# Kernel tuning notes

Measured on AMD Instinct MI355X. Metric: run time of the kernel, lower is better.

## Reference

```python
import jax, jax.numpy as jnp
import numpy as np

S, B, D, F = 2048, 8, 1024, 4096
EPS = 1e-5

def setup_inputs() -> dict:
    key = jax.random.key(0)
    ks = jax.random.split(key, 16)
    sc = lambda fan_in: 1.0 / np.sqrt(fan_in)
    inp = {
        'src': jax.random.normal(ks[0], (S, B, D), dtype=jnp.float32),
        'wq': jax.random.uniform(ks[1], (D, D), jnp.float32, -sc(D), sc(D)),
        'bq': jnp.zeros((D,), jnp.float32),
        'wk': jax.random.uniform(ks[2], (D, D), jnp.float32, -sc(D), sc(D)),
        'bk': jnp.zeros((D,), jnp.float32),
        'wv': jax.random.uniform(ks[3], (D, D), jnp.float32, -sc(D), sc(D)),
        'bv': jnp.zeros((D,), jnp.float32),
        'wo': jax.random.uniform(ks[4], (D, D), jnp.float32, -sc(D), sc(D)),
        'bo': jnp.zeros((D,), jnp.float32),
        'w1': jax.random.uniform(ks[5], (F, D), jnp.float32, -sc(D), sc(D)),
        'b1': jnp.zeros((F,), jnp.float32),
        'w2': jax.random.uniform(ks[6], (D, F), jnp.float32, -sc(F), sc(F)),
        'b2': jnp.zeros((D,), jnp.float32),
        'g1': jnp.ones((D,), jnp.float32),
        'be1': jnp.zeros((D,), jnp.float32),
        'g2': jnp.ones((D,), jnp.float32),
        'be2': jnp.zeros((D,), jnp.float32),
    }
    return inp

def _layer_norm(x, g, b):
    mu = jnp.mean(x, axis=-1, keepdims=True)
    var = jnp.mean(jnp.square(x - mu), axis=-1, keepdims=True)
    return (x - mu) / jnp.sqrt(var + EPS) * g + b

def _forward(src, wq, bq, wk, bk, wv, bv, wo, bo, w1, b1, w2, b2, g1, be1, g2, be2):
    # Linear attention (ELU+1 feature map, no normalizer — faithful to source)
    Q = jax.nn.elu(src @ wq.T + bq) + 1.0  # [S,B,D]
    K = jax.nn.elu(src @ wk.T + bk) + 1.0  # [S,B,D]
    V = src @ wv.T + bv                    # [S,B,D]
    KV = jnp.einsum('sbd,sbe->bde', K, V)  # [B,D,D]
    attn = jnp.einsum('sbd,bde->sbe', Q, KV)  # [S,B,D]
    attn = attn @ wo.T + bo
    x = _layer_norm(src + attn, g1, be1)   # dropout is identity (p=0 / eval)
    ffn = jax.nn.relu(x @ w1.T + b1) @ w2.T + b2
    return _layer_norm(x + ffn, g2, be2)

def reference(src, wq, bq, wk, bk, wv, bv, wo, bo, w1, b1, w2, b2, g1, be1, g2, be2):
    return _forward(src, wq, bq, wk, bk, wv, bv, wo, bo, w1, b1, w2, b2, g1, be1, g2, be2)
```

## Files before the change

### kernel.cpp

```cpp
#include <hip/hip_runtime.h>
#include <hip/hip_bf16.h>
#include <math.h>


typedef __attribute__((ext_vector_type(8))) short short8;
typedef __attribute__((ext_vector_type(4))) short short4_t;
typedef __attribute__((ext_vector_type(4))) float f32x4;

#define S_DIM 2048
#define B_DIM 8
#define D_DIM 1024
#define F_DIM 4096

__device__ __forceinline__ unsigned short f2bf(float f) {
  __hip_bfloat16 h = __float2bfloat16(f);
  return *reinterpret_cast<unsigned short*>(&h);
}
__device__ __forceinline__ float bf2f(unsigned short u) {
  return __bfloat162float(*reinterpret_cast<const __hip_bfloat16*>(&u));
}

#define GLD16(gp, sp)                                              \
  __builtin_amdgcn_global_load_lds(                                \
      (const __attribute__((address_space(1))) void*)(gp),         \
      (__attribute__((address_space(3))) void*)(sp), 16, 0, 0)

#define BAR()                                  \
  do {                                         \
    asm volatile("" ::: "memory");             \
    __builtin_amdgcn_s_barrier();              \
    asm volatile("" ::: "memory");             \
  } while (0)
#define WAITVM6() asm volatile("s_waitcnt vmcnt(6)" ::: "memory")
#define WAITVM10() asm volatile("s_waitcnt vmcnt(10)" ::: "memory")
#define WAITVM0() asm volatile("s_waitcnt vmcnt(0)" ::: "memory")

template <int EPI>
__global__ __launch_bounds__(512, 2) void gemm256_kernel(
    const unsigned short* __restrict__ A, long lda, long sA,
    const unsigned short* __restrict__ B, long ldb, long sB,
    void* __restrict__ Cv, long ldc, long sC,
    const float* __restrict__ bias,
    const void* __restrict__ residv, long ldr, long sR, int K) {
  __shared__ short lds[65536];
  const int gx = gridDim.x;
  const int nwg = gx * gridDim.y;
  const int orig = blockIdx.y * gx + blockIdx.x;
  const int cpx = nwg >> 3;
  const int wgid = (orig & 7) * cpx + (orig >> 3);
  const int bx = wgid % gx, by = wgid / gx;
  const int bz = blockIdx.z;
  const unsigned short* Ablk = A + (long)bz * sA + (long)by * 256 * lda;
  const unsigned short* Bblk = B + (long)bz * sB + (long)bx * 256 * ldb;

  const int tid = threadIdx.x;
  const int w = tid >> 6, lane = tid & 63;
  const int wm = w >> 2, wn = w & 3;
  const int lr = lane & 15, kh = lane >> 4;

  const int sr = w * 8 + (lane >> 3);
  const int sc = ((lane & 7) ^ (lane >> 3)) * 8;
  const int br0 = sr + ((sr >> 5) << 5);
  const unsigned short* pA = Ablk + (long)sr * lda + sc;
  const unsigned short* pB = Bblk + (long)br0 * ldb + sc;
  const long dA1 = 128 * lda, dAh = 64 * lda;
  const long dB1 = 128 * ldb, dBh = 32 * ldb;
  const int dst0 = w * 1024;
  const int dst1 = (8 + w) * 1024;

#define STAGE_A(bufOff, h, rel)                                               \
  do {                                                                        \
    GLD16(pA + (h) * dAh + (rel) * 64,                                        \
          (char*)lds + (bufOff) + (h)*16384 + dst0);                          \
    GLD16(pA + (h) * dAh + dA1 + (rel) * 64,                                  \
          (char*)lds + (bufOff) + (h)*16384 + dst1);                          \
  } while (0)
#define STAGE_B(bufOff, nh, rel)                                              \
  do {                                                                        \
    GLD16(pB + (nh) * dBh + (rel) * 64,                                       \
          (char*)lds + (bufOff) + 32768 + (nh)*16384 + dst0);                 \
    GLD16(pB + (nh) * dBh + dB1 + (rel) * 64,                                 \
          (char*)lds + (bufOff) + 32768 + (nh)*16384 + dst1);                 \
  } while (0)

  const int chk0 = ((kh ^ (lr & 7)) << 4);
  const int chk1 = (((4 + kh) ^ (lr & 7)) << 4);
  const int aRdBase = (wm * 64 + lr) * 128;
  const int bRdBase = (wn * 32 + lr) * 128;

  short8 af[4][2], b0r[2][2], b1r[2][2];
  f32x4 acc[8][4];
#pragma unroll
  for (int m = 0; m < 8; ++m)
#pragma unroll
    for (int n = 0; n < 4; ++n)
#pragma unroll
      for (int j = 0; j < 4; ++j) acc[m][n][j] = 0.f;

#define LDA_H(bufOff, h)                                                     \
  do {                                                                       \
    const char* _p = (const char*)lds + (bufOff) + (h)*16384 + aRdBase;      \
    _Pragma("unroll") for (int m = 0; m < 4; ++m) {                          \
      af[m][0] = *(const short8*)(_p + m * 2048 + chk0);                     \
      af[m][1] = *(const short8*)(_p + m * 2048 + chk1);                     \
    }                                                                        \
  } while (0)
#define LDB_H(dst, bufOff, nh)                                               \
  do {                                                                       \
    const char* _p = (const char*)lds + (bufOff) + 32768 + (nh)*16384 + bRdBase; \
    _Pragma("unroll") for (int n = 0; n < 2; ++n) {                          \
      dst[n][0] = *(const short8*)(_p + n * 2048 + chk0);                    \
      dst[n][1] = *(const short8*)(_p + n * 2048 + chk1);                    \
    }                                                                        \
  } while (0)
#define MFMA_Q(mh, nh, bset)                                                 \
  do {                                                                       \
    __builtin_amdgcn_s_setprio(1);                                           \
    _Pragma("unroll") for (int ks = 0; ks < 2; ++ks)                         \
    _Pragma("unroll") for (int m = 0; m < 4; ++m)                            \
    _Pragma("unroll") for (int n = 0; n < 2; ++n)                            \
      acc[(mh)*4 + m][(nh)*2 + n] = __builtin_amdgcn_mfma_f32_16x16x32_bf16( \
          af[m][ks], bset[n][ks], acc[(mh)*4 + m][(nh)*2 + n], 0, 0, 0);     \
    __builtin_amdgcn_s_setprio(0);                                           \
  } while (0)

  const int T = K >> 6;
  STAGE_A(0, 0, 0); STAGE_B(0, 0, 0); STAGE_B(0, 1, 0); STAGE_A(0, 1, 0);
  STAGE_A(65536, 0, 1); STAGE_B(65536, 0, 1); STAGE_B(65536, 1, 1);
  WAITVM10(); BAR();
  LDB_H(b0r, 0, 0);

  for (int i = 0; i < (T >> 1) - 1; ++i) {
    LDA_H(0, 0); STAGE_A(65536, 1, 1);
    BAR(); MFMA_Q(0, 0, b0r); BAR();
    LDB_H(b1r, 0, 1); STAGE_A(0, 0, 2);
    BAR(); MFMA_Q(0, 1, b1r); BAR();
    LDA_H(0, 1); STAGE_B(0, 0, 2);
    BAR(); MFMA_Q(1, 1, b1r); BAR();
    STAGE_B(0, 1, 2);
    WAITVM6(); BAR(); MFMA_Q(1, 0, b0r); LDB_H(b0r, 65536, 0); BAR();
    LDA_H(65536, 0); STAGE_A(0, 1, 2);
    BAR(); MFMA_Q(0, 0, b0r); BAR();
    LDB_H(b1r, 65536, 1); STAGE_A(65536, 0, 3);
    BAR(); MFMA_Q(0, 1, b1r); BAR();
    LDA_H(65536, 1); STAGE_B(65536, 0, 3);
    BAR(); MFMA_Q(1, 1, b1r); BAR();
    STAGE_B(65536, 1, 3);
    WAITVM6(); BAR(); MFMA_Q(1, 0, b0r); LDB_H(b0r, 0, 0); BAR();
    pA += 128; pB += 128;
  }

  LDA_H(0, 0); STAGE_A(65536, 1, 1);
  BAR(); MFMA_Q(0, 0, b0r); BAR();
  LDB_H(b1r, 0, 1);
  BAR(); MFMA_Q(0, 1, b1r); BAR();
  LDA_H(0, 1);
  BAR(); MFMA_Q(1, 1, b1r); BAR();
  WAITVM0(); BAR(); MFMA_Q(1, 0, b0r); LDB_H(b0r, 65536, 0); BAR();
  LDA_H(65536, 0);
  BAR(); MFMA_Q(0, 0, b0r); BAR();
  LDB_H(b1r, 65536, 1);
  BAR(); MFMA_Q(0, 1, b1r); BAR();
  LDA_H(65536, 1);
  BAR(); MFMA_Q(1, 1, b1r); BAR();
  MFMA_Q(1, 0, b0r);

  const long gm0 = (long)by * 256 + wm * 128;
  const long gn0 = (long)bx * 256 + wn * 64;
  if constexpr (EPI == 7) {
    unsigned short* C = (unsigned short*)Cv + (long)bz * sC;
    const float* R = (const float*)residv + (long)bz * sR;
#pragma unroll
    for (int mg = 0; mg < 8; ++mg)
#pragma unroll
      for (int ng = 0; ng < 4; ++ng) {
        const long col = gn0 + ng * 16 + lr;
        const float bcol = bias[col];
#pragma unroll
        for (int j = 0; j < 4; ++j) {
          const long row = gm0 + mg * 16 + kh * 4 + j;
          C[row * ldc + col] = f2bf(acc[mg][ng][j] + bcol + R[row * ldr + col]);
        }
      }
  } else if constexpr (EPI == 8) {
    unsigned short* C = (unsigned short*)Cv + (long)bz * sC;
    const unsigned short* R = (const unsigned short*)residv + (long)bz * sR;
#pragma unroll
    for (int mg = 0; mg < 8; ++mg)
#pragma unroll
      for (int ng = 0; ng < 4; ++ng) {
        const long col = gn0 + ng * 16 + lr;
        const float bcol = bias[col];
#pragma unroll
        for (int j = 0; j < 4; ++j) {
          const long row = gm0 + mg * 16 + kh * 4 + j;
          C[row * ldc + col] =
              f2bf(acc[mg][ng][j] + bcol + bf2f(R[row * ldr + col]));
        }
      }
  } else {
    unsigned short* C = (unsigned short*)Cv + (long)bz * sC;
    const bool do_elu = (EPI == 5) && (gn0 < 2048);
#pragma unroll
    for (int mg = 0; mg < 8; ++mg)
#pragma unroll
      for (int ng = 0; ng < 4; ++ng) {
        const long col = gn0 + ng * 16 + lr;
        float bcol = 0.f;
        if constexpr (EPI != 0) bcol = bias[col];
#pragma unroll
        for (int j = 0; j < 4; ++j) {
          const long row = gm0 + mg * 16 + kh * 4 + j;
          float v = acc[mg][ng][j] + bcol;
          if constexpr (EPI == 3) v = fmaxf(v, 0.f);
          if constexpr (EPI == 5) {
            if (do_elu) v = (v > 0.f) ? (v + 1.f) : expf(v);
          }
          C[row * ldc + col] = f2bf(v);
        }
      }
  }
#undef STAGE_A
#undef STAGE_B
#undef LDA_H
#undef LDB_H
#undef MFMA_Q
}

__global__ __launch_bounds__(256) void transpose_kernel(
    const unsigned short* __restrict__ inbase,
    unsigned short* __restrict__ outbase, long ld) {
  __shared__ unsigned short t[64][68];
  const int z = blockIdx.z;
  const int which = z >> 3, b = z & 7;
  const unsigned short* in = inbase + (which ? 2048 : 1024);
  unsigned short* out = outbase + (long)which * 16777216L;
  const long s0 = (long)blockIdx.x * 64, d0 = (long)blockIdx.y * 64;
  const int tid = threadIdx.x;
  {
    const int r = tid >> 3, c = (tid & 7) * 8;
#pragma unroll
    for (int it = 0; it < 2; ++it) {
      const int s = r + it * 32;
      const unsigned short* g = &in[((s0 + s) * B_DIM + b) * ld + d0 + c];
      short4_t v0 = *(const short4_t*)g;
      short4_t v1 = *(const short4_t*)(g + 4);
      *(short4_t*)&t[s][c] = v0;
      *(short4_t*)&t[s][c + 4] = v1;
    }
  }
  __syncthreads();
  {
    const int d = tid >> 3, c = (tid & 7) * 8;
#pragma unroll
    for (int it = 0; it < 2; ++it) {
      const int dd = d + it * 32;
      short8 v;
#pragma unroll
      for (int j = 0; j < 8; ++j) v[j] = (short)t[c + j][dd];
      *(short8*)&out[(long)b * ((long)D_DIM * S_DIM) + (d0 + dd) * S_DIM + s0 + c] = v;
    }
  }
}

template <int OUT_FP32>
__global__ __launch_bounds__(256) void layernorm_bf_kernel(
    const unsigned short* __restrict__ in, void* __restrict__ outv,
    const float* __restrict__ gamma, const float* __restrict__ beta) {
  const long row = blockIdx.x;
  const int tid = threadIdx.x;
  const int lane = tid & 63, w = tid >> 6;
  short4_t r4 = *(const short4_t*)&in[row * D_DIM + tid * 4];
  f32x4 v;
#pragma unroll
  for (int j = 0; j < 4; ++j) v[j] = bf2f((unsigned short)r4[j]);
  float s = v[0] + v[1] + v[2] + v[3];
  float q = v[0] * v[0] + v[1] * v[1] + v[2] * v[2] + v[3] * v[3];
#pragma unroll
  for (int off = 32; off > 0; off >>= 1) {
    s += __shfl_down(s, off, 64);
    q += __shfl_down(q, off, 64);
  }
  __shared__ float red[8];
  if (lane == 0) { red[w] = s; red[w + 4] = q; }
  __syncthreads();
  s = red[0] + red[1] + red[2] + red[3];
  q = red[4] + red[5] + red[6] + red[7];
  const float mu = s * (1.f / D_DIM);
  const float var = q * (1.f / D_DIM) - mu * mu;
  const float rs = rsqrtf(var + 1e-5f);
  f32x4 g = *(const f32x4*)&gamma[tid * 4];
  f32x4 bb = *(const f32x4*)&beta[tid * 4];
  if constexpr (OUT_FP32) {
    f32x4 o;
#pragma unroll
    for (int j = 0; j < 4; ++j) o[j] = (v[j] - mu) * rs * g[j] + bb[j];
    *(f32x4*)&((float*)outv)[row * D_DIM + tid * 4] = o;
  } else {
    short4_t ob;
#pragma unroll
    for (int j = 0; j < 4; ++j)
      ob[j] = (short)f2bf((v[j] - mu) * rs * g[j] + bb[j]);
    *(short4_t*)&((unsigned short*)outv)[row * D_DIM + tid * 4] = ob;
  }
}

__global__ __launch_bounds__(256) void cast_all_kernel(
    const float* __restrict__ wq, const float* __restrict__ wk,
    const float* __restrict__ wv, const float* __restrict__ wo,
    const float* __restrict__ w1, const float* __restrict__ w2,
    const float* __restrict__ src,
    unsigned short* __restrict__ wqkvb, unsigned short* __restrict__ wob,
    unsigned short* __restrict__ w1b, unsigned short* __restrict__ w2b,
    unsigned short* __restrict__ srcb) {
  int b = blockIdx.x;
  const float* in;
  unsigned short* out;
  if (b < 512)        { in = wq;  out = wqkvb;           }
  else if (b < 1024)  { in = wk;  out = wqkvb + 1048576; b -= 512;  }
  else if (b < 1536)  { in = wv;  out = wqkvb + 2097152; b -= 1024; }
  else if (b < 2048)  { in = wo;  out = wob;             b -= 1536; }
  else if (b < 4096)  { in = w1;  out = w1b;             b -= 2048; }
  else if (b < 6144)  { in = w2;  out = w2b;             b -= 4096; }
  else                { in = src; out = srcb;            b -= 6144; }
  const long i = ((long)b * 256 + threadIdx.x) * 8;
  f32x4 a = *(const f32x4*)&in[i];
  f32x4 c = *(const f32x4*)&in[i + 4];
  short8 v;
#pragma unroll
  for (int j = 0; j < 4; ++j) v[j] = (short)f2bf(a[j]);
#pragma unroll
  for (int j = 0; j < 4; ++j) v[4 + j] = (short)f2bf(c[j]);
  *(short8*)&out[i] = v;
}

__global__ __launch_bounds__(1024) void copy3_kernel(
    const float* __restrict__ bq, const float* __restrict__ bk,
    const float* __restrict__ bv, float* __restrict__ bqkv) {
  const float* s = blockIdx.x == 0 ? bq : (blockIdx.x == 1 ? bk : bv);
  bqkv[blockIdx.x * 1024 + threadIdx.x] = s[threadIdx.x];
}

extern "C" void kernel_launch(void* const* d_in, const int* in_sizes, int n_in,
                              void* d_out, int out_size, void* d_ws, size_t ws_size,
                              hipStream_t stream) {
  const float* src = (const float*)d_in[0];
  const float* wq  = (const float*)d_in[1];
  const float* bq  = (const float*)d_in[2];
  const float* wk  = (const float*)d_in[3];
  const float* bk  = (const float*)d_in[4];
  const float* wv  = (const float*)d_in[5];
  const float* bv  = (const float*)d_in[6];
  const float* wo  = (const float*)d_in[7];
  const float* bo  = (const float*)d_in[8];
  const float* w1  = (const float*)d_in[9];
  const float* b1  = (const float*)d_in[10];
  const float* w2  = (const float*)d_in[11];
  const float* b2  = (const float*)d_in[12];
  const float* g1  = (const float*)d_in[13];
  const float* be1 = (const float*)d_in[14];
  const float* g2  = (const float*)d_in[15];
  const float* be2 = (const float*)d_in[16];

  const long MB = 1024L * 1024L;
  if (ws_size < 248 * MB) return;
  char* ws = (char*)d_ws;
  unsigned short* w1b   = (unsigned short*)(ws + 0 * MB);
  unsigned short* w2b   = (unsigned short*)(ws + 8 * MB);
  unsigned short* srcb  = (unsigned short*)(ws + 16 * MB);
  unsigned short* Kt    = (unsigned short*)(ws + 16 * MB);
  unsigned short* AOb   = (unsigned short*)(ws + 16 * MB);
  unsigned short* Yb    = (unsigned short*)(ws + 16 * MB);
  unsigned short* Xb    = (unsigned short*)(ws + 48 * MB);
  unsigned short* KVm   = (unsigned short*)(ws + 80 * MB);
  unsigned short* Mt    = (unsigned short*)(ws + 96 * MB);
  unsigned short* wqkvb = (unsigned short*)(ws + 112 * MB);
  float*          bqkv  = (float*)(ws + 118 * MB);
  unsigned short* wob   = (unsigned short*)(ws + 119 * MB);
  unsigned short* QKVb  = (unsigned short*)(ws + 144 * MB);
  unsigned short* H     = (unsigned short*)(ws + 112 * MB);

  const dim3 blk(256);
  const dim3 blk512(512);
  cast_all_kernel<<<dim3(14336), blk, 0, stream>>>(
      wq, wk, wv, wo, w1, w2, src, wqkvb, wob, w1b, w2b, srcb);
  copy3_kernel<<<dim3(3), dim3(1024), 0, stream>>>(bq, bk, bv, bqkv);

  gemm256_kernel<5><<<dim3(12, 64, 1), blk512, 0, stream>>>(
      srcb, 1024, 0, wqkvb, 1024, 0, QKVb, 3072, 0, bqkv, nullptr, 0, 0, 1024);

  transpose_kernel<<<dim3(32, 16, 16), blk, 0, stream>>>(QKVb, Kt, 3072);

  gemm256_kernel<0><<<dim3(4, 4, 8), blk512, 0, stream>>>(
      Kt, 2048, 2097152, Kt + 16777216L, 2048, 2097152, KVm, 1024, 1048576,
      nullptr, nullptr, 0, 0, 2048);
  gemm256_kernel<0><<<dim3(4, 4, 8), blk512, 0, stream>>>(
      wob, 1024, 0, KVm, 1024, 1048576, Mt, 1024, 1048576,
      nullptr, nullptr, 0, 0, 1024);
  gemm256_kernel<7><<<dim3(4, 8, 8), blk512, 0, stream>>>(
      QKVb, 24576, 3072, Mt, 1024, 1048576, AOb, 8192, 1024,
      bo, src, 8192, 1024, 1024);

  layernorm_bf_kernel<0><<<dim3(16384), blk, 0, stream>>>(AOb, Xb, g1, be1);

  gemm256_kernel<3><<<dim3(16, 64, 1), blk512, 0, stream>>>(
      Xb, 1024, 0, w1b, 1024, 0, H, 4096, 0, b1, nullptr, 0, 0, 1024);
  gemm256_kernel<8><<<dim3(4, 64, 1), blk512, 0, stream>>>(
      H, 4096, 0, w2b, 4096, 0, Yb, 1024, 0, b2, Xb, 1024, 0, 4096);

  layernorm_bf_kernel<1><<<dim3(16384), blk, 0, stream>>>(
      Yb, (float*)d_out, g2, be2);
}
```

Baseline: 590.0 us.

## Reschedule GEMM main loop to overlap LDS fragment loads with MFMA

Reorders the 256x256 GEMM main loop so LDS-to-register fragment loads (LDA_H/LDB_H) are issued alongside MFMA quarters instead of in their own barrier-separated phases. It also adds finer vmcnt waits before barriers and removes most barriers from the epilogue tail. The aim is to hide LDS read latency behind matrix math and cut barrier stalls. The risk is reading LDS regions that async global_load_lds writes have not finished filling, or overwriting fragments still in use, if the wait counts or buffer ordering are wrong.

```diff
diff --git a/kernel.cpp b/kernel.cpp
--- a/kernel.cpp
+++ b/kernel.cpp
@@ -31,7 +31,7 @@
     __builtin_amdgcn_s_barrier();              \
     asm volatile("" ::: "memory");             \
   } while (0)
-#define WAITVM6() asm volatile("s_waitcnt vmcnt(6)" ::: "memory")
+#define WAITVM8() asm volatile("s_waitcnt vmcnt(8)" ::: "memory")
 #define WAITVM10() asm volatile("s_waitcnt vmcnt(10)" ::: "memory")
 #define WAITVM0() asm volatile("s_waitcnt vmcnt(0)" ::: "memory")
 
@@ -128,41 +128,68 @@
   STAGE_A(0, 0, 0); STAGE_B(0, 0, 0); STAGE_B(0, 1, 0); STAGE_A(0, 1, 0);
   STAGE_A(65536, 0, 1); STAGE_B(65536, 0, 1); STAGE_B(65536, 1, 1);
   WAITVM10(); BAR();
+  LDA_H(0, 0);
   LDB_H(b0r, 0, 0);
 
   for (int i = 0; i < (T >> 1) - 1; ++i) {
-    LDA_H(0, 0); STAGE_A(65536, 1, 1);
-    BAR(); MFMA_Q(0, 0, b0r); BAR();
-    LDB_H(b1r, 0, 1); STAGE_A(0, 0, 2);
-    BAR(); MFMA_Q(0, 1, b1r); BAR();
-    LDA_H(0, 1); STAGE_B(0, 0, 2);
-    BAR(); MFMA_Q(1, 1, b1r); BAR();
+    STAGE_A(65536, 1, 1);
+    WAITVM10(); BAR();
+    LDB_H(b1r, 0, 1);
+    MFMA_Q(0, 0, b0r);
+    BAR();
+    STAGE_A(0, 0, 2);
+    WAITVM10(); BAR();
+    MFMA_Q(0, 1, b1r);
+    LDA_H(0, 1);
+    BAR();
+    STAGE_B(0, 0, 2);
+    BAR();
+    MFMA_Q(1, 1, b1r);
+    BAR();
     STAGE_B(0, 1, 2);
-    WAITVM6(); BAR(); MFMA_Q(1, 0, b0r); LDB_H(b0r, 65536, 0); BAR();
-    LDA_H(65536, 0); STAGE_A(0, 1, 2);
-    BAR(); MFMA_Q(0, 0, b0r); BAR();
-    LDB_H(b1r, 65536, 1); STAGE_A(65536, 0, 3);
-    BAR(); MFMA_Q(0, 1, b1r); BAR();
-    LDA_H(65536, 1); STAGE_B(65536, 0, 3);
-    BAR(); MFMA_Q(1, 1, b1r); BAR();
+    WAITVM8(); BAR();
+    LDB_H(b1r, 65536, 1);
+    MFMA_Q(1, 0, b0r);
+    LDA_H(65536, 0);
+    LDB_H(b0r, 65536, 0);
+    BAR();
+    STAGE_A(0, 1, 2);
+    BAR();
+    MFMA_Q(0, 0, b0r);
+    BAR();
+    STAGE_A(65536, 0, 3);
+    WAITVM10(); BAR();
+    MFMA_Q(0, 1, b1r);
+    LDA_H(65536, 1);
+    BAR();
+    STAGE_B(65536, 0, 3);
+    BAR();
+    MFMA_Q(1, 1, b1r);
+    BAR();
     STAGE_B(65536, 1, 3);
-    WAITVM6(); BAR(); MFMA_Q(1, 0, b0r); LDB_H(b0r, 0, 0); BAR();
+    WAITVM10(); BAR();
+    MFMA_Q(1, 0, b0r);
+    LDA_H(0, 0);
+    LDB_H(b0r, 0, 0);
+    BAR();
     pA += 128; pB += 128;
   }
 
-  LDA_H(0, 0); STAGE_A(65536, 1, 1);
-  BAR(); MFMA_Q(0, 0, b0r); BAR();
+  STAGE_A(65536, 1, 1);
+  WAITVM0(); BAR();
   LDB_H(b1r, 0, 1);
-  BAR(); MFMA_Q(0, 1, b1r); BAR();
+  MFMA_Q(0, 0, b0r);
+  MFMA_Q(0, 1, b1r);
   LDA_H(0, 1);
-  BAR(); MFMA_Q(1, 1, b1r); BAR();
-  WAITVM0(); BAR(); MFMA_Q(1, 0, b0r); LDB_H(b0r, 65536, 0); BAR();
+  MFMA_Q(1, 1, b1r);
+  MFMA_Q(1, 0, b0r);
   LDA_H(65536, 0);
-  BAR(); MFMA_Q(0, 0, b0r); BAR();
+  LDB_H(b0r, 65536, 0);
   LDB_H(b1r, 65536, 1);
-  BAR(); MFMA_Q(0, 1, b1r); BAR();
+  MFMA_Q(0, 0, b0r);
+  MFMA_Q(0, 1, b1r);
   LDA_H(65536, 1);
-  BAR(); MFMA_Q(1, 1, b1r); BAR();
+  MFMA_Q(1, 1, b1r);
   MFMA_Q(1, 0, b0r);
 
   const long gm0 = (long)by * 256 + wm * 128;
```

Measured after the change: 857.0 us. 1.45x slower.
